# Kernel optimization log

Hardware: AMD Instinct MI355X
Metric: run time of the kernel (lower is better)

The kernel has to match this reference:

```python
import jax, jax.numpy as jnp
import numpy as np

B = 8          # batch
HID = 1024     # hidden_size
NH = 8         # query heads
KVH = 1        # kv heads (GQA)
HD = 256       # head_dim
NL = 18        # layers
MLP = 4096     # intermediate size
AH = 50        # action_horizon (suffix len)
AD = 32        # action_dim
P = 1037       # prefix_len
EPS = 1e-6
ROPE_BASE = 10000.0
SCALE = HD ** -0.5
NEG = -2.3819763e38


def _rms(x):
    return x * jax.lax.rsqrt(jnp.mean(x * x, axis=-1, keepdims=True) + EPS)


def _ada_norm(x, cond, W):
    # AdaRMS: cond -> (scale, shift, gate); normed*(1+scale)+shift, gate returned for gated residual
    scale, shift, gate = jnp.split(cond @ W, 3, axis=-1)
    return _rms(x) * (1.0 + scale[:, None, :]) + shift[:, None, :], gate[:, None, :]


def _rope(x, pos):
    # x: [B, heads, S, HD], pos: [B, S]; HF rotate-half convention
    inv = 1.0 / (ROPE_BASE ** (jnp.arange(0, HD, 2, dtype=jnp.float32) / HD))
    freqs = pos[:, :, None].astype(jnp.float32) * inv          # [B,S,HD/2]
    cos = jnp.tile(jnp.cos(freqs), (1, 1, 2))[:, None]          # [B,1,S,HD]
    sin = jnp.tile(jnp.sin(freqs), (1, 1, 2))[:, None]
    x1, x2 = jnp.split(x, 2, axis=-1)
    return x * cos + jnp.concatenate([-x2, x1], axis=-1) * sin


def setup_inputs() -> dict:
    key = jax.random.key(0)
    ks = jax.random.split(key, 24)
    s = 0.02
    return {
        'prefix_keys': jax.random.normal(ks[0], (B, NL, KVH, P, HD), jnp.float32),
        'prefix_values': jax.random.normal(ks[1], (B, NL, KVH, P, HD), jnp.float32),
        'prefix_pad_masks': jnp.ones((B, P), dtype=bool),
        'x_t': jax.random.normal(ks[2], (B, AH, AD), jnp.float32),
        'timestep': jax.random.uniform(ks[3], (B,), jnp.float32),
        'Wq': jax.random.normal(ks[4], (NL, HID, NH * HD), jnp.float32) * s,
        'Wk': jax.random.normal(ks[5], (NL, HID, KVH * HD), jnp.float32) * s,
        'Wv': jax.random.normal(ks[6], (NL, HID, KVH * HD), jnp.float32) * s,
        'Wo': jax.random.normal(ks[7], (NL, NH * HD, HID), jnp.float32) * s,
        'Wg': jax.random.normal(ks[8], (NL, HID, MLP), jnp.float32) * s,
        'Wu': jax.random.normal(ks[9], (NL, HID, MLP), jnp.float32) * s,
        'Wd': jax.random.normal(ks[10], (NL, MLP, HID), jnp.float32) * s,
        'A1': jax.random.normal(ks[11], (NL, HID, 3 * HID), jnp.float32) * s,
        'A2': jax.random.normal(ks[12], (NL, HID, 3 * HID), jnp.float32) * s,
        'Af': jax.random.normal(ks[13], (HID, 3 * HID), jnp.float32) * s,
        'W_act_in': jax.random.normal(ks[14], (AD, HID), jnp.float32) * s,
        'b_act_in': jnp.zeros((HID,), jnp.float32),
        'W_act_out': jax.random.normal(ks[15], (HID, AD), jnp.float32) * s,
        'b_act_out': jnp.zeros((AD,), jnp.float32),
        'W_t_in': jax.random.normal(ks[16], (HID, HID), jnp.float32) * s,
        'b_t_in': jnp.zeros((HID,), jnp.float32),
        'W_t_out': jax.random.normal(ks[17], (HID, HID), jnp.float32) * s,
        'b_t_out': jnp.zeros((HID,), jnp.float32),
    }


def reference(prefix_keys, prefix_values, prefix_pad_masks, x_t, timestep,
              Wq, Wk, Wv, Wo, Wg, Wu, Wd, A1, A2, Af,
              W_act_in, b_act_in, W_act_out, b_act_out,
              W_t_in, b_t_in, W_t_out, b_t_out):
    b = x_t.shape[0]
    # --- time embedding (sinusoidal over log-spaced periods) -> AdaRMS cond ---
    frac = jnp.linspace(0.0, 1.0, HID // 2)
    period = 0.004 * (4.0 / 0.004) ** frac
    sin_in = (2.0 * jnp.pi / period)[None, :] * timestep[:, None]
    temb = jnp.concatenate([jnp.sin(sin_in), jnp.cos(sin_in)], axis=1)  # [B,HID]
    cond = jax.nn.silu(jax.nn.silu(temb @ W_t_in + b_t_in) @ W_t_out + b_t_out)

    # --- action input projection ---
    h = x_t @ W_act_in + b_act_in  # [B,AH,HID]

    # --- attention mask & positions ---
    # suffix att_masks = [1,0,...,0] -> cumsum constant -> suffix block fully visible
    suf_att = jnp.ones((b, AH, AH), dtype=bool)
    s2p = jnp.broadcast_to(prefix_pad_masks[:, None, :], (b, AH, P))
    full = jnp.concatenate([s2p, suf_att], axis=2)          # [B,AH,P+AH]
    bias = jnp.where(full, 0.0, NEG).astype(jnp.float32)[:, None]  # [B,1,AH,P+AH]
    offs = jnp.sum(prefix_pad_masks.astype(jnp.int32), axis=-1, keepdims=True)
    pos = offs + jnp.arange(AH)                              # [B,AH]

    def layer(hcur, p):
        wq, wk, wv, wo, wg, wu, wd, a1, a2, ck, cv = p
        normed, gate = _ada_norm(hcur, cond, a1)
        q = (normed @ wq).reshape(b, AH, NH, HD).transpose(0, 2, 1, 3)
        k = (normed @ wk).reshape(b, AH, KVH, HD).transpose(0, 2, 1, 3)
        v = (normed @ wv).reshape(b, AH, KVH, HD).transpose(0, 2, 1, 3)
        q = _rope(q, pos)
        k = _rope(k, pos)
        fk = jnp.concatenate([ck, k], axis=2)   # [B,KVH,P+AH,HD]
        fv = jnp.concatenate([cv, v], axis=2)
        rep = NH // KVH
        fk = jnp.repeat(fk, rep, axis=1)
        fv = jnp.repeat(fv, rep, axis=1)
        scores = jnp.einsum('bhqd,bhkd->bhqk', q, fk) * SCALE + bias
        attn = jax.nn.softmax(scores, axis=-1)
        o = jnp.einsum('bhqk,bhkd->bhqd', attn, fv)
        o = o.transpose(0, 2, 1, 3).reshape(b, AH, NH * HD) @ wo
        h1 = hcur + gate * o                     # gated residual 1
        n2, gate2 = _ada_norm(h1, cond, a2)
        mlp = (jax.nn.gelu(n2 @ wg, approximate=True) * (n2 @ wu)) @ wd
        return h1 + gate2 * mlp, None            # gated residual 2

    pk = jnp.moveaxis(prefix_keys, 1, 0)   # [NL,B,KVH,P,HD]
    pv = jnp.moveaxis(prefix_values, 1, 0)
    h, _ = jax.lax.scan(layer, h, (Wq, Wk, Wv, Wo, Wg, Wu, Wd, A1, A2, pk, pv))

    out, _ = _ada_norm(h, cond, Af)
    return out @ W_act_out + b_act_out  # [B,AH,AD]
```

## Files before the change

kernel.cpp:

```cpp
#include <hip/hip_runtime.h>

typedef unsigned short u16;
typedef unsigned int   u32;
typedef __attribute__((ext_vector_type(8))) short bh8;
typedef __attribute__((ext_vector_type(4))) float f4;

constexpr int BATCH = 8, HIDN = 1024, NHEAD = 8, HD = 256, NLAY = 18, DMLP = 4096;
constexpr int AHOR = 50, ADIMN = 32, PFXN = 1037, SEQN = 1087, NSTR = 17, MR = 400, MP = 512;
constexpr float EPSV = 1e-6f, NEGV = -2.3819763e38f, QSCALE = 0.0625f;
constexpr size_t ADASL = (size_t)37 * 3 * BATCH * HIDN;

static __device__ __forceinline__ u16 f2bf(float x){
  union{float f; u32 u;} v; v.f = x;
  u32 r = (v.u + 0x7FFFu + ((v.u >> 16) & 1u)) >> 16;
  return (u16)r;
}
static __device__ __forceinline__ float bf2f(u16 u){
  union{u32 u; float f;} v; v.u = ((u32)u) << 16; return v.f;
}
static __device__ __forceinline__ u32 pack2(float a, float b){
  return (u32)f2bf(a) | ((u32)f2bf(b) << 16);
}
static __device__ __forceinline__ f4 MFMA(bh8 a, bh8 b, f4 c){
  return __builtin_amdgcn_mfma_f32_16x16x32_bf16(a, b, c, 0, 0, 0);
}
static __device__ __forceinline__ float siluf_(float x){ return x / (1.f + __expf(-x)); }
static __device__ __forceinline__ float geluf_(float x){
  float y = 0.7978845608028654f * (x + 0.044715f * x * x * x);
  float e = __expf(2.f * y);
  return 0.5f * x * (2.f - 2.f / (e + 1.f));
}

__global__ void k_prep(const int* __restrict__ mask, const float* __restrict__ ts,
                       float* __restrict__ temb, int* __restrict__ offs,
                       float* __restrict__ ropec, float* __restrict__ ropes)
{
  int t = threadIdx.x;
  {
    int b = t >> 5, l = t & 31;
    const int* mp = mask + b * PFXN;
    int s = 0;
    for (int k = l; k < PFXN; k += 32) s += (mp[k] != 0);
    #pragma unroll
    for (int off = 16; off >= 1; off >>= 1) s += __shfl_xor(s, off);
    if (l == 0) offs[b] = s;
  }
  for (int i = t; i < BATCH * 512; i += 256){
    int b = i >> 9, j = i & 511;
    float frac = (float)j * (1.0f / 511.0f);
    float period = 0.004f * __expf(frac * 6.907755278982137f);
    float arg = (6.283185307179586f / period) * ts[b];
    float s, c; sincosf(arg, &s, &c);
    temb[b * HIDN + j] = s;
    temb[b * HIDN + 512 + j] = c;
  }
  __syncthreads();
  for (int i = t; i < BATCH * AHOR * 128; i += 256){
    int d = i & 127, bt = i >> 7, b = bt / AHOR, tt = bt % AHOR;
    float inv = __expf(-((float)d * (1.f / 128.f)) * 9.210340371976184f);
    float arg = (float)(offs[b] + tt) * inv;
    float s, c; sincosf(arg, &s, &c);
    ropec[i] = c; ropes[i] = s;
  }
}

__global__ void k_tproj(const float* __restrict__ X, const float* __restrict__ W,
                        const float* __restrict__ bias, float* __restrict__ out)
{
  __shared__ float xs[BATCH * HIDN];
  __shared__ float red[BATCH][8][32];
  int t = threadIdx.x;
  for (int i = t; i < BATCH * HIDN; i += 256) xs[i] = X[i];
  __syncthreads();
  int c = t & 31, kp = t >> 5;
  int c0 = blockIdx.x * 32;
  float acc[BATCH];
  #pragma unroll
  for (int b = 0; b < BATCH; ++b) acc[b] = 0.f;
  for (int k = kp * 128; k < kp * 128 + 128; ++k){
    float w = W[(size_t)k * HIDN + c0 + c];
    #pragma unroll
    for (int b = 0; b < BATCH; ++b) acc[b] += xs[b * HIDN + k] * w;
  }
  #pragma unroll
  for (int b = 0; b < BATCH; ++b) red[b][kp][c] = acc[b];
  __syncthreads();
  int b2 = t >> 5, c2 = t & 31;
  float s = bias[c0 + c2];
  #pragma unroll
  for (int kp2 = 0; kp2 < 8; ++kp2) s += red[b2][kp2][c2];
  out[b2 * HIDN + c0 + c2] = siluf_(s);
}

__global__ void k_ada_part(const float* __restrict__ cond, const float* __restrict__ A1,
                           const float* __restrict__ A2, const float* __restrict__ Af,
                           float* __restrict__ adap)
{
  __shared__ float cs[BATCH * 256];
  int t = threadIdx.x;
  int y = blockIdx.y, ks = blockIdx.z;
  int k0 = ks * 256;
  for (int i = t; i < BATCH * 256; i += 256){
    int b = i >> 8, kk = i & 255;
    cs[i] = cond[b * HIDN + k0 + kk];
  }
  __syncthreads();
  const float* A = (y < NLAY) ? (A1 + (size_t)y * HIDN * 3072)
                  : (y < 2 * NLAY) ? (A2 + (size_t)(y - NLAY) * HIDN * 3072) : Af;
  int n = (blockIdx.x * 256 + t) * 4;
  f4 acc[BATCH];
  #pragma unroll
  for (int b = 0; b < BATCH; ++b) acc[b] = (f4){0.f,0.f,0.f,0.f};
  const float* ap = A + (size_t)k0 * 3072 + n;
  for (int kk = 0; kk < 256; kk += 8){
    f4 av[8];
    #pragma unroll
    for (int j = 0; j < 8; ++j) av[j] = *(const f4*)(ap + (size_t)(kk + j) * 3072);
    #pragma unroll
    for (int j = 0; j < 8; ++j){
      #pragma unroll
      for (int b = 0; b < BATCH; ++b) acc[b] += av[j] * cs[b * 256 + kk + j];
    }
  }
  int comp = n >> 10, nn = n & 1023;
  float* o = adap + (size_t)ks * ADASL + ((size_t)y * 3 + comp) * BATCH * HIDN + nn;
  #pragma unroll
  for (int b = 0; b < BATCH; ++b) *(f4*)(o + b * HIDN) = acc[b];
}

__global__ void k_ada_red(const float* __restrict__ adap, float* __restrict__ ada)
{
  size_t i = ((size_t)blockIdx.x * 256 + threadIdx.x) * 8;
  f4 a0 = {0,0,0,0}, a1 = {0,0,0,0};
  #pragma unroll
  for (int ks = 0; ks < 4; ++ks){
    const float* p = adap + (size_t)ks * ADASL + i;
    a0 += *(const f4*)p;
    a1 += *(const f4*)(p + 4);
  }
  *(f4*)(ada + i) = a0;
  *(f4*)(ada + i + 4) = a1;
}

__global__ void k_hin(const float* __restrict__ xt, const float* __restrict__ W,
                      const float* __restrict__ bias, float* __restrict__ h)
{
  int r = blockIdx.x;
  int t = threadIdx.x; int c0 = t * 4;
  __shared__ float xs[ADIMN];
  if (t < ADIMN) xs[t] = xt[r * ADIMN + t];
  __syncthreads();
  float a0 = bias[c0], a1 = bias[c0+1], a2 = bias[c0+2], a3 = bias[c0+3];
  for (int k = 0; k < ADIMN; ++k){
    float x = xs[k];
    const float* wp = W + k * HIDN + c0;
    a0 += x * wp[0]; a1 += x * wp[1]; a2 += x * wp[2]; a3 += x * wp[3];
  }
  float* hp = h + (size_t)r * HIDN + c0;
  hp[0] = a0; hp[1] = a1; hp[2] = a2; hp[3] = a3;
}

__global__ void k_resnorm(int mode, int np,
    const float* __restrict__ base, const u16* __restrict__ parts,
    const float* __restrict__ gate, const float* __restrict__ sc,
    const float* __restrict__ sh, float* __restrict__ outres,
    u16* __restrict__ fragA)
{
  __shared__ float redl[4];
  int t = threadIdx.x;
  int c = t * 4;
  for (int i = 0; i < 4; ++i){
    int r = blockIdx.x * 4 + i;
    bool live = (r < MR);
    float4 v = {0.f,0.f,0.f,0.f};
    int b = live ? (r / AHOR) : 0;
    if (live){
      v = *(const float4*)(base + (size_t)r * HIDN + c);
      if (mode){
        float s0 = 0, s1 = 0, s2 = 0, s3 = 0;
        #pragma unroll 4
        for (int p = 0; p < np; ++p){
          ushort4 u4 = *(const ushort4*)(parts + ((size_t)p * MP + r) * HIDN + c);
          s0 += bf2f(u4.x); s1 += bf2f(u4.y); s2 += bf2f(u4.z); s3 += bf2f(u4.w);
        }
        float4 gp = *(const float4*)(gate + b * HIDN + c);
        v.x += gp.x * s0; v.y += gp.y * s1; v.z += gp.z * s2; v.w += gp.w * s3;
        *(float4*)(outres + (size_t)r * HIDN + c) = v;
      }
    }
    float ss = v.x*v.x + v.y*v.y + v.z*v.z + v.w*v.w;
    #pragma unroll
    for (int off = 1; off < 64; off <<= 1) ss += __shfl_xor(ss, off);
    if ((t & 63) == 0) redl[t >> 6] = ss;
    __syncthreads();
    float tot = redl[0] + redl[1] + redl[2] + redl[3];
    __syncthreads();
    u16* dst = fragA + ((size_t)(c >> 3)) * MP * 8 + (size_t)r * 8 + (c & 7);
    ushort4 ov;
    if (live){
      float rstd = rsqrtf(tot * (1.0f / HIDN) + EPSV);
      const float4 scp = *(const float4*)(sc + b * HIDN + c);
      const float4 shp = *(const float4*)(sh + b * HIDN + c);
      ov.x = f2bf(v.x * rstd * (1.f + scp.x) + shp.x);
      ov.y = f2bf(v.y * rstd * (1.f + scp.y) + shp.y);
      ov.z = f2bf(v.z * rstd * (1.f + scp.z) + shp.z);
      ov.w = f2bf(v.w * rstd * (1.f + scp.w) + shp.w);
    } else {
      ov.x = ov.y = ov.z = ov.w = 0;
    }
    *(ushort4*)dst = ov;
  }
}

template<int NOUTER>
static __device__ __forceinline__ void gemm_core64(
    const u16* __restrict__ fa,
    const float* __restrict__ Wa, int cb0,
    const float* __restrict__ Wb, int cb1,
    int wN, int kc0, u16* lds, f4 acc[4][4])
{
  const int tid = threadIdx.x;
  const int lane = tid & 63, wave = tid >> 6;
  const int l15 = lane & 15, g = lane >> 4;
  const int wrow = wave * 64;
  const int sn = tid & 63, skb = (tid >> 6) * 8;
  const float* wbase = (sn < 32) ? (Wa + cb0 + sn) : (Wb + cb1 + (sn - 32));
  const size_t krow0 = (size_t)kc0 * 8 + skb;
  float pre[3][8];
  bh8 ab[2][2][4];
  #pragma unroll
  for (int j = 0; j < 8; ++j) pre[0][j] = wbase[(krow0 + j) * wN];
  #pragma unroll
  for (int kk = 0; kk < 2; ++kk){
    const u16* ap = fa + ((size_t)(kc0 + kk * 4 + g) * MP + wrow + l15) * 8;
    #pragma unroll
    for (int mf = 0; mf < 4; ++mf) ab[0][kk][mf] = *(const bh8*)(ap + mf * 128);
  }
  if (NOUTER > 1){
    #pragma unroll
    for (int j = 0; j < 8; ++j) pre[1][j] = wbase[(krow0 + 64 + j) * wN];
  }
  if (NOUTER > 2){
    #pragma unroll
    for (int j = 0; j < 8; ++j) pre[2][j] = wbase[(krow0 + 128 + j) * wN];
  }
  { u32* dst = (u32*)(lds + sn * 88 + skb);
    dst[0] = pack2(pre[0][0], pre[0][1]); dst[1] = pack2(pre[0][2], pre[0][3]);
    dst[2] = pack2(pre[0][4], pre[0][5]); dst[3] = pack2(pre[0][6], pre[0][7]); }
  __syncthreads();
  #pragma unroll
  for (int ko = 0; ko < NOUTER; ++ko){
    u16* ldsr = lds + (ko & 1) * (64 * 88);
    if (ko + 1 < NOUTER){
      #pragma unroll
      for (int kk = 0; kk < 2; ++kk){
        const u16* ap = fa + ((size_t)(kc0 + (ko + 1) * 8 + kk * 4 + g) * MP + wrow + l15) * 8;
        #pragma unroll
        for (int mf = 0; mf < 4; ++mf) ab[(ko + 1) & 1][kk][mf] = *(const bh8*)(ap + mf * 128);
      }
    }
    if (ko + 3 < NOUTER){
      #pragma unroll
      for (int j = 0; j < 8; ++j) pre[ko % 3][j] = wbase[(krow0 + (size_t)(ko + 3) * 64 + j) * wN];
    }
    #pragma unroll
    for (int kk = 0; kk < 2; ++kk){
      bh8 bb[4];
      #pragma unroll
      for (int nf = 0; nf < 4; ++nf) bb[nf] = *(const bh8*)(ldsr + (nf * 16 + l15) * 88 + kk * 32 + g * 8);
      #pragma unroll
      for (int mf = 0; mf < 4; ++mf)
        #pragma unroll
        for (int nf = 0; nf < 4; ++nf)
          acc[mf][nf] = MFMA(ab[ko & 1][kk][mf], bb[nf], acc[mf][nf]);
    }
    if (ko + 1 < NOUTER){
      u16* ldsw = lds + ((ko + 1) & 1) * (64 * 88);
      u32* dst = (u32*)(ldsw + sn * 88 + skb);
      const float* p = pre[(ko + 1) % 3];
      dst[0] = pack2(p[0], p[1]); dst[1] = pack2(p[2], p[3]);
      dst[2] = pack2(p[4], p[5]); dst[3] = pack2(p[6], p[7]);
      __syncthreads();
    }
  }
}

template<int NOUTER>
static __device__ __forceinline__ void gemm_core32w(
    const u16* __restrict__ fa,
    const float* __restrict__ Wa, int cb0,
    const float* __restrict__ Wb, int cb1,
    int wN, u16* lds, f4 acc[4][2])
{
  const int tid = threadIdx.x;
  const int lane = tid & 63, wave = tid >> 6;
  const int l15 = lane & 15, g = lane >> 4;
  const int wrow = wave * 64;
  const int sc = tid & 31, kq = tid >> 5;
  const int kb = kq * 8;
  const float* wbase = (sc < 16) ? (Wa + cb0 + sc) : (Wb + cb1 + (sc - 16));
  float pre[3][8];
  #pragma unroll
  for (int j = 0; j < 8; ++j) pre[0][j] = wbase[(size_t)(kb + j) * wN];
  if (NOUTER > 1){
    #pragma unroll
    for (int j = 0; j < 8; ++j) pre[1][j] = wbase[(size_t)(128 + kb + j) * wN];
  }
  if (NOUTER > 2){
    #pragma unroll
    for (int j = 0; j < 8; ++j) pre[2][j] = wbase[(size_t)(256 + kb + j) * wN];
  }
  { u32* dst = (u32*)(lds + sc * 136 + kb);
    dst[0] = pack2(pre[0][0], pre[0][1]); dst[1] = pack2(pre[0][2], pre[0][3]);
    dst[2] = pack2(pre[0][4], pre[0][5]); dst[3] = pack2(pre[0][6], pre[0][7]); }
  __syncthreads();
  #pragma unroll
  for (int ko = 0; ko < NOUTER; ++ko){
    u16* ldsr = lds + (ko & 1) * (32 * 136);
    bh8 a01[2][4], a23[2][4];
    #pragma unroll
    for (int kk = 0; kk < 2; ++kk){
      const u16* ap = fa + ((size_t)(ko * 16 + kk * 4 + g) * MP + wrow + l15) * 8;
      #pragma unroll
      for (int mf = 0; mf < 4; ++mf) a01[kk][mf] = *(const bh8*)(ap + mf * 128);
    }
    if (ko + 3 < NOUTER){
      #pragma unroll
      for (int j = 0; j < 8; ++j) pre[ko % 3][j] = wbase[(size_t)((ko + 3) * 128 + kb + j) * wN];
    }
    #pragma unroll
    for (int kk = 2; kk < 4; ++kk){
      const u16* ap = fa + ((size_t)(ko * 16 + kk * 4 + g) * MP + wrow + l15) * 8;
      #pragma unroll
      for (int mf = 0; mf < 4; ++mf) a23[kk - 2][mf] = *(const bh8*)(ap + mf * 128);
    }
    #pragma unroll
    for (int kk = 0; kk < 2; ++kk){
      bh8 bb[2];
      #pragma unroll
      for (int nf = 0; nf < 2; ++nf) bb[nf] = *(const bh8*)(ldsr + (nf * 16 + l15) * 136 + kk * 32 + g * 8);
      #pragma unroll
      for (int mf = 0; mf < 4; ++mf){
        acc[mf][0] = MFMA(a01[kk][mf], bb[0], acc[mf][0]);
        acc[mf][1] = MFMA(a01[kk][mf], bb[1], acc[mf][1]);
      }
    }
    #pragma unroll
    for (int kk = 2; kk < 4; ++kk){
      bh8 bb[2];
      #pragma unroll
      for (int nf = 0; nf < 2; ++nf) bb[nf] = *(const bh8*)(ldsr + (nf * 16 + l15) * 136 + kk * 32 + g * 8);
      #pragma unroll
      for (int mf = 0; mf < 4; ++mf){
        acc[mf][0] = MFMA(a23[kk - 2][mf], bb[0], acc[mf][0]);
        acc[mf][1] = MFMA(a23[kk - 2][mf], bb[1], acc[mf][1]);
      }
    }
    if (ko + 1 < NOUTER){
      u16* ldsw = lds + ((ko + 1) & 1) * (32 * 136);
      u32* dst = (u32*)(ldsw + sc * 136 + kb);
      const float* p = pre[(ko + 1) % 3];
      dst[0] = pack2(p[0], p[1]); dst[1] = pack2(p[2], p[3]);
      dst[2] = pack2(p[4], p[5]); dst[3] = pack2(p[6], p[7]);
      __syncthreads();
    }
  }
}

__global__ __launch_bounds__(512) void k_qkvrope(
    const u16* __restrict__ n1, const float* __restrict__ Wq,
    const float* __restrict__ Wk, const float* __restrict__ Wv,
    const float* __restrict__ ropec, const float* __restrict__ ropes,
    u16* __restrict__ qf, u16* __restrict__ ks, u16* __restrict__ vs)
{
  __shared__ u16 lds[2 * 64 * 88];
  int bx = blockIdx.x;
  const float* Wa; int cb0, cb1, wN, head = 0, d0 = 0, type;
  if (bx < 32){ type = 0; head = bx >> 2; d0 = (bx & 3) * 32; Wa = Wq; wN = NHEAD * HD; cb0 = head * HD + d0; cb1 = cb0 + 128; }
  else if (bx < 36){ type = 1; d0 = (bx - 32) * 32; Wa = Wk; wN = HD; cb0 = d0; cb1 = d0 + 128; }
  else { type = 2; d0 = (bx - 36) * 64; Wa = Wv; wN = HD; cb0 = d0; cb1 = cb0 + 32; }
  f4 acc[4][4];
  #pragma unroll
  for (int i = 0; i < 4; ++i)
    #pragma unroll
    for (int j = 0; j < 4; ++j) acc[i][j] = (f4){0.f, 0.f, 0.f, 0.f};
  gemm_core64<16>(n1, Wa, cb0, Wa, cb1, wN, 0, lds, acc);
  int tid = threadIdx.x, lane = tid & 63, wave = tid >> 6, l15 = lane & 15, g = lane >> 4;
  int wrow = wave * 64;
  #pragma unroll
  for (int mf = 0; mf < 4; ++mf)
    #pragma unroll
    for (int r = 0; r < 4; ++r){
      int row = wrow + mf * 16 + 4 * g + r;
      if (row >= MR) continue;
      int b = row / AHOR, tt = row - b * AHOR;
      if (type == 2){
        #pragma unroll
        for (int nf = 0; nf < 4; ++nf){
          int d = d0 + nf * 16 + l15;
          vs[((size_t)(b * AHOR + tt)) * HD + d] = f2bf(acc[mf][nf][r]);
        }
      } else {
        #pragma unroll
        for (int nf = 0; nf < 2; ++nf){
          int dA = d0 + nf * 16 + l15;
          float cz = ropec[(size_t)(b * AHOR + tt) * 128 + dA];
          float sz = ropes[(size_t)(b * AHOR + tt) * 128 + dA];
          float a = acc[mf][nf][r], bv = acc[mf][nf + 2][r];
          float oA = a * cz - bv * sz;
          float oB = bv * cz + a * sz;
          if (type == 0){
            oA *= QSCALE; oB *= QSCALE;
            int rowp = head * AHOR + tt;
            int dB = dA + 128;
            qf[((size_t)(b * 32 + (dA >> 3))) * MP * 8 + (size_t)rowp * 8 + (dA & 7)] = f2bf(oA);
            qf[((size_t)(b * 32 + (dB >> 3))) * MP * 8 + (size_t)rowp * 8 + (dB & 7)] = f2bf(oB);
          } else {
            size_t kb = ((size_t)(b * AHOR + tt)) * HD;
            ks[kb + dA] = f2bf(oA);
            ks[kb + dA + 128] = f2bf(oB);
          }
        }
      }
    }
}

__global__ __launch_bounds__(512) void k_attn(
    const u16* __restrict__ qf, const u16* __restrict__ kss, const u16* __restrict__ vss,
    const float* __restrict__ pk, const float* __restrict__ pv,
    const int* __restrict__ mask, int layer,
    u16* __restrict__ opart, float* __restrict__ mrow, float* __restrict__ lrow)
{
  __shared__ u16 kv[256 * 88];
  __shared__ u16 plds[MP * 72];
  int s = blockIdx.x, b = blockIdx.y;
  int tid = threadIdx.x, lane = tid & 63, wave = tid >> 6, l15 = lane & 15, g = lane >> 4;
  int wrow = wave * 64;
  int key = tid >> 3, dblk = (tid & 7) * 32;
  int kg = s * 64 + key;
  {
    u32* dst = (u32*)(kv + key * 264 + dblk);
    if (kg < PFXN){
      const float4* src = (const float4*)(pk + (((size_t)b * NLAY + layer) * PFXN + kg) * HD + dblk);
      #pragma unroll
      for (int j = 0; j < 8; ++j){ float4 v = src[j]; dst[2*j] = pack2(v.x, v.y); dst[2*j+1] = pack2(v.z, v.w); }
    } else if (kg < SEQN){
      const u32* src = (const u32*)(kss + ((size_t)b * AHOR + (kg - PFXN)) * HD + dblk);
      #pragma unroll
      for (int j = 0; j < 16; ++j) dst[j] = src[j];
    } else {
      #pragma unroll
      for (int j = 0; j < 16; ++j) dst[j] = 0;
    }
  }
  float vreg[32];
  if (kg < PFXN){
    const float4* src = (const float4*)(pv + (((size_t)b * NLAY + layer) * PFXN + kg) * HD + dblk);
    #pragma unroll
    for (int j = 0; j < 8; ++j){ float4 v = src[j]; vreg[4*j] = v.x; vreg[4*j+1] = v.y; vreg[4*j+2] = v.z; vreg[4*j+3] = v.w; }
  } else if (kg < SEQN){
    const u32* src = (const u32*)(vss + ((size_t)b * AHOR + (kg - PFXN)) * HD + dblk);
    #pragma unroll
    for (int j = 0; j < 16; ++j){ u32 u = src[j]; vreg[2*j] = bf2f((u16)(u & 0xFFFF)); vreg[2*j+1] = bf2f((u16)(u >> 16)); }
  } else {
    #pragma unroll
    for (int j = 0; j < 32; ++j) vreg[j] = 0.f;
  }
  bool valid[4];
  #pragma unroll
  for (int nf = 0; nf < 4; ++nf){
    int kgc = s * 64 + nf * 16 + l15;
    valid[nf] = (kgc < PFXN) ? (mask[b * PFXN + kgc] != 0) : (kgc < SEQN);
  }
  __syncthreads();
  f4 acc[4][4];
  #pragma unroll
  for (int i = 0; i < 4; ++i)
    #pragma unroll
    for (int j = 0; j < 4; ++j) acc[i][j] = (f4){0.f,0.f,0.f,0.f};
  const u16* qb = qf + (size_t)b * 32 * MP * 8;
  #pragma unroll
  for (int ko = 0; ko < 4; ++ko)
    #pragma unroll
    for (int kk = 0; kk < 2; ++kk){
      int kc = ko * 8 + kk * 4 + g;
      bh8 a[4], bb[4];
      const u16* ap = qb + ((size_t)kc * MP + wrow + l15) * 8;
      #pragma unroll
      for (int mf = 0; mf < 4; ++mf) a[mf] = *(const bh8*)(ap + mf * 128);
      #pragma unroll
      for (int nf = 0; nf < 4; ++nf) bb[nf] = *(const bh8*)(kv + (nf * 16 + l15) * 264 + ko * 64 + kk * 32 + g * 8);
      #pragma unroll
      for (int mf = 0; mf < 4; ++mf)
        #pragma unroll
        for (int nf = 0; nf < 4; ++nf) acc[mf][nf] = MFMA(a[mf], bb[nf], acc[mf][nf]);
    }
  #pragma unroll
  for (int nf = 0; nf < 4; ++nf) if (!valid[nf]){
    #pragma unroll
    for (int mf = 0; mf < 4; ++mf){
      acc[mf][nf][0] = NEGV; acc[mf][nf][1] = NEGV; acc[mf][nf][2] = NEGV; acc[mf][nf][3] = NEGV;
    }
  }
  #pragma unroll
  for (int mf = 0; mf < 4; ++mf)
    #pragma unroll
    for (int r = 0; r < 4; ++r){
      float m0 = fmaxf(fmaxf(acc[mf][0][r], acc[mf][1][r]), fmaxf(acc[mf][2][r], acc[mf][3][r]));
      #pragma unroll
      for (int off = 1; off < 16; off <<= 1) m0 = fmaxf(m0, __shfl_xor(m0, off));
      int row = wrow + mf * 16 + 4 * g + r;
      float sum = 0.f;
      #pragma unroll
      for (int nf = 0; nf < 4; ++nf){
        float p = __expf(acc[mf][nf][r] - m0);
        sum += p;
        plds[row * 72 + nf * 16 + l15] = f2bf(p);
      }
      #pragma unroll
      for (int off = 1; off < 16; off <<= 1) sum += __shfl_xor(sum, off);
      if (l15 == 0){
        mrow[((size_t)b * NSTR + s) * MP + row] = m0;
        lrow[((size_t)b * NSTR + s) * MP + row] = sum;
      }
    }
  __syncthreads();
  {
    #pragma unroll
    for (int j = 0; j < 32; ++j){
      int d = dblk + j;
      kv[d * 88 + ((d >> 5) & 3) * 8 + key] = f2bf(vreg[j]);
    }
  }
  __syncthreads();
  #pragma unroll
  for (int dc = 0; dc < 4; ++dc){
    f4 oc[4][4];
    #pragma unroll
    for (int i = 0; i < 4; ++i)
      #pragma unroll
      for (int j = 0; j < 4; ++j) oc[i][j] = (f4){0.f,0.f,0.f,0.f};
    #pragma unroll
    for (int kk = 0; kk < 2; ++kk){
      bh8 a[4], bb[4];
      #pragma unroll
      for (int mf = 0; mf < 4; ++mf) a[mf] = *(const bh8*)(plds + (wrow + mf * 16 + l15) * 72 + kk * 32 + g * 8);
      #pragma unroll
      for (int nf = 0; nf < 4; ++nf){
        int dcol = dc * 64 + nf * 16 + l15;
        bb[nf] = *(const bh8*)(kv + dcol * 88 + ((dcol >> 5) & 3) * 8 + kk * 32 + g * 8);
      }
      #pragma unroll
      for (int mf = 0; mf < 4; ++mf)
        #pragma unroll
        for (int nf = 0; nf < 4; ++nf) oc[mf][nf] = MFMA(a[mf], bb[nf], oc[mf][nf]);
    }
    #pragma unroll
    for (int mf = 0; mf < 4; ++mf)
      #pragma unroll
      for (int r = 0; r < 4; ++r){
        int row = wrow + mf * 16 + 4 * g + r;
        if (row < MR){
          #pragma unroll
          for (int nf = 0; nf < 4; ++nf){
            int d = dc * 64 + nf * 16 + l15;
            opart[(((size_t)b * NSTR + s) * MR + row) * HD + d] = f2bf(oc[mf][nf][r]);
          }
        }
      }
  }
}

__global__ void k_comb(const u16* __restrict__ opart, const float* __restrict__ mrow,
                       const float* __restrict__ lrow, u16* __restrict__ ao)
{
  int b = blockIdx.y;
  int d = threadIdx.x;
  int r0 = blockIdx.x * 16;
  for (int i = 0; i < 16; ++i){
    int row = r0 + i;
    float M = -3.0e38f;
    for (int s2 = 0; s2 < NSTR; ++s2) M = fmaxf(M, mrow[((size_t)b * NSTR + s2) * MP + row]);
    float L = 0.f, o = 0.f;
    for (int s2 = 0; s2 < NSTR; ++s2){
      float w = __expf(mrow[((size_t)b * NSTR + s2) * MP + row] - M);
      L += w * lrow[((size_t)b * NSTR + s2) * MP + row];
      o += w * bf2f(opart[(((size_t)b * NSTR + s2) * MR + row) * HD + d]);
    }
    float val = o / L;
    int h = row / AHOR, tt = row - h * AHOR;
    int col = h * HD + d;
    int rg = b * AHOR + tt;
    ao[((size_t)(col >> 3)) * MP * 8 + (size_t)rg * 8 + (col & 7)] = f2bf(val);
  }
}

template<int NOUTER>
__global__ __launch_bounds__(512) void k_gemm_part(
    const u16* __restrict__ fa, const float* __restrict__ W, int wN,
    int kcPerSlice, u16* __restrict__ outp)
{
  __shared__ u16 lds[2 * 64 * 88];
  int n0 = blockIdx.x * 64;
  int ksl = blockIdx.y;
  f4 acc[4][4];
  #pragma unroll
  for (int i = 0; i < 4; ++i)
    #pragma unroll
    for (int j = 0; j < 4; ++j) acc[i][j] = (f4){0.f,0.f,0.f,0.f};
  gemm_core64<NOUTER>(fa, W, n0, W, n0 + 32, wN, ksl * kcPerSlice, lds, acc);
  int tid = threadIdx.x, lane = tid & 63, wave = tid >> 6, l15 = lane & 15, g = lane >> 4;
  int wrow = wave * 64;
  #pragma unroll
  for (int mf = 0; mf < 4; ++mf)
    #pragma unroll
    for (int r = 0; r < 4; ++r){
      int row = wrow + mf * 16 + 4 * g + r;
      #pragma unroll
      for (int nf = 0; nf < 4; ++nf)
        outp[((size_t)ksl * MP + row) * 1024 + n0 + nf * 16 + l15] = f2bf(acc[mf][nf][r]);
    }
}

__global__ __launch_bounds__(512) void k_mlpup(
    const u16* __restrict__ n2, const float* __restrict__ Wg, const float* __restrict__ Wu,
    u16* __restrict__ mlpf)
{
  __shared__ u16 lds[2 * 32 * 136];
  int n0 = blockIdx.x * 16;
  f4 acc[4][2];
  #pragma unroll
  for (int i = 0; i < 4; ++i)
    #pragma unroll
    for (int j = 0; j < 2; ++j) acc[i][j] = (f4){0.f,0.f,0.f,0.f};
  gemm_core32w<8>(n2, Wg, n0, Wu, n0, DMLP, lds, acc);
  int tid = threadIdx.x, lane = tid & 63, wave = tid >> 6, l15 = lane & 15, g = lane >> 4;
  int wrow = wave * 64;
  #pragma unroll
  for (int mf = 0; mf < 4; ++mf)
    #pragma unroll
    for (int r = 0; r < 4; ++r){
      int row = wrow + mf * 16 + 4 * g + r;
      int col = n0 + l15;
      float gg = acc[mf][0][r], uu = acc[mf][1][r];
      float act = geluf_(gg) * uu;
      mlpf[((size_t)(col >> 3)) * MP * 8 + (size_t)row * 8 + (col & 7)] = f2bf(act);
    }
}

__global__ void k_out(const u16* __restrict__ nfr, const float* __restrict__ W,
                      const float* __restrict__ bias, float* __restrict__ out)
{
  int t = threadIdx.x;
  int row = blockIdx.x * 8 + (t >> 5);
  int c = t & 31;
  float acc = bias[c];
  for (int k = 0; k < HIDN; ++k)
    acc += bf2f(nfr[((size_t)(k >> 3)) * MP * 8 + (size_t)row * 8 + (k & 7)]) * W[k * ADIMN + c];
  out[row * ADIMN + c] = acc;
}

extern "C" void kernel_launch(void* const* d_in, const int* in_sizes, int n_in,
                              void* d_out, int out_size, void* d_ws, size_t ws_size,
                              hipStream_t stream)
{
  const float* pk  = (const float*)d_in[0];
  const float* pv  = (const float*)d_in[1];
  const int*   msk = (const int*)d_in[2];
  const float* xt  = (const float*)d_in[3];
  const float* ts  = (const float*)d_in[4];
  const float* Wq  = (const float*)d_in[5];
  const float* Wk  = (const float*)d_in[6];
  const float* Wv  = (const float*)d_in[7];
  const float* Wo  = (const float*)d_in[8];
  const float* Wg  = (const float*)d_in[9];
  const float* Wu  = (const float*)d_in[10];
  const float* Wd  = (const float*)d_in[11];
  const float* A1  = (const float*)d_in[12];
  const float* A2  = (const float*)d_in[13];
  const float* Af  = (const float*)d_in[14];
  const float* Wai = (const float*)d_in[15];
  const float* bai = (const float*)d_in[16];
  const float* Wao = (const float*)d_in[17];
  const float* bao = (const float*)d_in[18];
  const float* Wti = (const float*)d_in[19];
  const float* bti = (const float*)d_in[20];
  const float* Wto = (const float*)d_in[21];
  const float* bto = (const float*)d_in[22];

  char* w = (char*)d_ws;
  size_t off = 0;
  auto alloc = [&](size_t bytes) -> char* {
    char* p = w + off; off += (bytes + 255) & ~(size_t)255; return p;
  };
  float* temb  = (float*)alloc((size_t)BATCH * HIDN * 4);
  float* ttmp  = (float*)alloc((size_t)BATCH * HIDN * 4);
  float* cond  = (float*)alloc((size_t)BATCH * HIDN * 4);
  int*   offs  = (int*)alloc(BATCH * 4);
  float* ropec = (float*)alloc((size_t)BATCH * AHOR * 128 * 4);
  float* ropes = (float*)alloc((size_t)BATCH * AHOR * 128 * 4);
  float* ada   = (float*)alloc(ADASL * 4);
  float* adap  = (float*)alloc(4 * ADASL * 4);
  float* h     = (float*)alloc((size_t)MR * HIDN * 4);
  float* h1    = (float*)alloc((size_t)MR * HIDN * 4);
  u16*   n1    = (u16*)alloc((size_t)128 * MP * 8 * 2);
  u16*   n2    = (u16*)alloc((size_t)128 * MP * 8 * 2);
  u16*   qf    = (u16*)alloc((size_t)BATCH * 32 * MP * 8 * 2);
  u16*   kss   = (u16*)alloc((size_t)BATCH * AHOR * HD * 2);
  u16*   vss   = (u16*)alloc((size_t)BATCH * AHOR * HD * 2);
  u16*   opart = (u16*)alloc((size_t)BATCH * NSTR * MR * HD * 2);
  float* mrow  = (float*)alloc((size_t)BATCH * NSTR * MP * 4);
  float* lrow  = (float*)alloc((size_t)BATCH * NSTR * MP * 4);
  u16*   ao    = (u16*)alloc((size_t)256 * MP * 8 * 2);
  u16*   opp   = (u16*)alloc((size_t)8 * MP * 1024 * 2);
  u16*   mlpf  = (u16*)alloc((size_t)512 * MP * 8 * 2);
  u16*   mdp   = (u16*)alloc((size_t)8 * MP * 1024 * 2);
  if (off > ws_size) return;

  k_prep<<<1, 256, 0, stream>>>(msk, ts, temb, offs, ropec, ropes);
  k_tproj<<<32, 256, 0, stream>>>(temb, Wti, bti, ttmp);
  k_tproj<<<32, 256, 0, stream>>>(ttmp, Wto, bto, cond);
  k_ada_part<<<dim3(3, 37, 4), 256, 0, stream>>>(cond, A1, A2, Af, adap);
  k_ada_red<<<444, 256, 0, stream>>>(adap, ada);
  k_hin<<<MR, 256, 0, stream>>>(xt, Wai, bai, h);

  auto AP = [&](int y, int comp){ return ada + ((size_t)y * 3 + comp) * BATCH * HIDN; };

  k_resnorm<<<128, 256, 0, stream>>>(0, 0, h, nullptr, nullptr, AP(0,0), AP(0,1), nullptr, n1);

  for (int l = 0; l < NLAY; ++l){
    k_qkvrope<<<40, 512, 0, stream>>>(n1, Wq + (size_t)l * HIDN * NHEAD * HD,
                                      Wk + (size_t)l * HIDN * HD, Wv + (size_t)l * HIDN * HD,
                                      ropec, ropes, qf, kss, vss);
    k_attn<<<dim3(NSTR, BATCH), 512, 0, stream>>>(qf, kss, vss, pk, pv, msk, l, opart, mrow, lrow);
    k_comb<<<dim3(25, BATCH), 256, 0, stream>>>(opart, mrow, lrow, ao);
    k_gemm_part<4><<<dim3(16, 8), 512, 0, stream>>>(ao, Wo + (size_t)l * 2048 * 1024, 1024, 32, opp);
    k_resnorm<<<128, 256, 0, stream>>>(1, 8, h, opp, AP(l,2), AP(NLAY+l,0), AP(NLAY+l,1), h1, n2);
    k_mlpup<<<256, 512, 0, stream>>>(n2, Wg + (size_t)l * HIDN * DMLP, Wu + (size_t)l * HIDN * DMLP, mlpf);
    k_gemm_part<8><<<dim3(16, 8), 512, 0, stream>>>(mlpf, Wd + (size_t)l * DMLP * 1024, 1024, 64, mdp);
    const float* nsc = (l < NLAY - 1) ? AP(l + 1, 0) : AP(36, 0);
    const float* nsh = (l < NLAY - 1) ? AP(l + 1, 1) : AP(36, 1);
    k_resnorm<<<128, 256, 0, stream>>>(2, 8, h1, mdp, AP(NLAY+l,2), nsc, nsh, h, n1);
  }
  k_out<<<50, 256, 0, stream>>>(n1, Wao, bao, (float*)d_out);
}
```

Before: 3.532 ms.

## Split small kernels across more blocks to raise parallelism on the GPU

Several under-filled launches get more blocks. The ada-projection K-split goes from 4 to 8 parts. The QKV+RoPE GEMM goes from 40 to 80 blocks with narrower tiles via gemm_core32w. Attention is split over the head dimension in two z-halves, and the combine kernel goes from 25 to 100 blocks. The aim is better CU occupancy on a 256-CU device, at the cost of recomputing QK scores and softmax in both attention halves and loading K twice.

```diff
diff --git a/kernel.cpp b/kernel.cpp
--- a/kernel.cpp
+++ b/kernel.cpp
@@ -96,12 +96,12 @@
                            const float* __restrict__ A2, const float* __restrict__ Af,
                            float* __restrict__ adap)
 {
-  __shared__ float cs[BATCH * 256];
+  __shared__ float cs[BATCH * 128];
   int t = threadIdx.x;
   int y = blockIdx.y, ks = blockIdx.z;
-  int k0 = ks * 256;
-  for (int i = t; i < BATCH * 256; i += 256){
-    int b = i >> 8, kk = i & 255;
+  int k0 = ks * 128;
+  for (int i = t; i < BATCH * 128; i += 256){
+    int b = i >> 7, kk = i & 127;
     cs[i] = cond[b * HIDN + k0 + kk];
   }
   __syncthreads();
@@ -112,14 +112,14 @@
   #pragma unroll
   for (int b = 0; b < BATCH; ++b) acc[b] = (f4){0.f,0.f,0.f,0.f};
   const float* ap = A + (size_t)k0 * 3072 + n;
-  for (int kk = 0; kk < 256; kk += 8){
+  for (int kk = 0; kk < 128; kk += 8){
     f4 av[8];
     #pragma unroll
     for (int j = 0; j < 8; ++j) av[j] = *(const f4*)(ap + (size_t)(kk + j) * 3072);
     #pragma unroll
     for (int j = 0; j < 8; ++j){
       #pragma unroll
-      for (int b = 0; b < BATCH; ++b) acc[b] += av[j] * cs[b * 256 + kk + j];
+      for (int b = 0; b < BATCH; ++b) acc[b] += av[j] * cs[b * 128 + kk + j];
     }
   }
   int comp = n >> 10, nn = n & 1023;
@@ -133,7 +133,7 @@
   size_t i = ((size_t)blockIdx.x * 256 + threadIdx.x) * 8;
   f4 a0 = {0,0,0,0}, a1 = {0,0,0,0};
   #pragma unroll
-  for (int ks = 0; ks < 4; ++ks){
+  for (int ks = 0; ks < 8; ++ks){
     const float* p = adap + (size_t)ks * ADASL + i;
     a0 += *(const f4*)p;
     a1 += *(const f4*)(p + 4);
@@ -373,18 +373,18 @@
     const float* __restrict__ ropec, const float* __restrict__ ropes,
     u16* __restrict__ qf, u16* __restrict__ ks, u16* __restrict__ vs)
 {
-  __shared__ u16 lds[2 * 64 * 88];
+  __shared__ u16 lds[2 * 32 * 136];
   int bx = blockIdx.x;
-  const float* Wa; int cb0, cb1, wN, head = 0, d0 = 0, type;
-  if (bx < 32){ type = 0; head = bx >> 2; d0 = (bx & 3) * 32; Wa = Wq; wN = NHEAD * HD; cb0 = head * HD + d0; cb1 = cb0 + 128; }
-  else if (bx < 36){ type = 1; d0 = (bx - 32) * 32; Wa = Wk; wN = HD; cb0 = d0; cb1 = d0 + 128; }
-  else { type = 2; d0 = (bx - 36) * 64; Wa = Wv; wN = HD; cb0 = d0; cb1 = cb0 + 32; }
-  f4 acc[4][4];
+  const float *Wa, *Wb; int cb0, cb1, wN, type, head = 0, fb = 0, d0 = 0;
+  if (bx < 64){ type = 0; head = bx >> 3; fb = (bx & 7) * 16; Wa = Wq; Wb = Wq; wN = NHEAD * HD; cb0 = head * HD + fb; cb1 = cb0 + 128; }
+  else if (bx < 72){ type = 1; fb = (bx - 64) * 16; Wa = Wk; Wb = Wk; wN = HD; cb0 = fb; cb1 = fb + 128; }
+  else { type = 2; d0 = (bx - 72) * 32; Wa = Wv; Wb = Wv; wN = HD; cb0 = d0; cb1 = d0 + 16; }
+  f4 acc[4][2];
   #pragma unroll
   for (int i = 0; i < 4; ++i)
     #pragma unroll
-    for (int j = 0; j < 4; ++j) acc[i][j] = (f4){0.f, 0.f, 0.f, 0.f};
-  gemm_core64<16>(n1, Wa, cb0, Wa, cb1, wN, 0, lds, acc);
+    for (int j = 0; j < 2; ++j) acc[i][j] = (f4){0.f, 0.f, 0.f, 0.f};
+  gemm_core32w<8>(n1, Wa, cb0, Wb, cb1, wN, lds, acc);
   int tid = threadIdx.x, lane = tid & 63, wave = tid >> 6, l15 = lane & 15, g = lane >> 4;
   int wrow = wave * 64;
   #pragma unroll
@@ -394,32 +394,27 @@
       int row = wrow + mf * 16 + 4 * g + r;
       if (row >= MR) continue;
       int b = row / AHOR, tt = row - b * AHOR;
+      float lo = acc[mf][0][r], hi = acc[mf][1][r];
       if (type == 2){
-        #pragma unroll
-        for (int nf = 0; nf < 4; ++nf){
-          int d = d0 + nf * 16 + l15;
-          vs[((size_t)(b * AHOR + tt)) * HD + d] = f2bf(acc[mf][nf][r]);
-        }
+        size_t vb = ((size_t)(b * AHOR + tt)) * HD;
+        vs[vb + d0 + l15] = f2bf(lo);
+        vs[vb + d0 + 16 + l15] = f2bf(hi);
       } else {
-        #pragma unroll
-        for (int nf = 0; nf < 2; ++nf){
-          int dA = d0 + nf * 16 + l15;
-          float cz = ropec[(size_t)(b * AHOR + tt) * 128 + dA];
-          float sz = ropes[(size_t)(b * AHOR + tt) * 128 + dA];
-          float a = acc[mf][nf][r], bv = acc[mf][nf + 2][r];
-          float oA = a * cz - bv * sz;
-          float oB = bv * cz + a * sz;
-          if (type == 0){
-            oA *= QSCALE; oB *= QSCALE;
-            int rowp = head * AHOR + tt;
-            int dB = dA + 128;
-            qf[((size_t)(b * 32 + (dA >> 3))) * MP * 8 + (size_t)rowp * 8 + (dA & 7)] = f2bf(oA);
-            qf[((size_t)(b * 32 + (dB >> 3))) * MP * 8 + (size_t)rowp * 8 + (dB & 7)] = f2bf(oB);
-          } else {
-            size_t kb = ((size_t)(b * AHOR + tt)) * HD;
-            ks[kb + dA] = f2bf(oA);
-            ks[kb + dA + 128] = f2bf(oB);
-          }
+        int dA = fb + l15;
+        float cz = ropec[(size_t)(b * AHOR + tt) * 128 + dA];
+        float sz = ropes[(size_t)(b * AHOR + tt) * 128 + dA];
+        float oA = lo * cz - hi * sz;
+        float oB = hi * cz + lo * sz;
+        if (type == 0){
+          oA *= QSCALE; oB *= QSCALE;
+          int rowp = head * AHOR + tt;
+          int dB = dA + 128;
+          qf[((size_t)(b * 32 + (dA >> 3))) * MP * 8 + (size_t)rowp * 8 + (dA & 7)] = f2bf(oA);
+          qf[((size_t)(b * 32 + (dB >> 3))) * MP * 8 + (size_t)rowp * 8 + (dB & 7)] = f2bf(oB);
+        } else {
+          size_t kb = ((size_t)(b * AHOR + tt)) * HD;
+          ks[kb + dA] = f2bf(oA);
+          ks[kb + dA + 128] = f2bf(oB);
         }
       }
     }
@@ -431,14 +426,14 @@
     const int* __restrict__ mask, int layer,
     u16* __restrict__ opart, float* __restrict__ mrow, float* __restrict__ lrow)
 {
-  __shared__ u16 kv[256 * 88];
+  __shared__ u16 kv[64 * 264];
   __shared__ u16 plds[MP * 72];
-  int s = blockIdx.x, b = blockIdx.y;
+  int s = blockIdx.x, b = blockIdx.y, z = blockIdx.z;
   int tid = threadIdx.x, lane = tid & 63, wave = tid >> 6, l15 = lane & 15, g = lane >> 4;
   int wrow = wave * 64;
-  int key = tid >> 3, dblk = (tid & 7) * 32;
-  int kg = s * 64 + key;
   {
+    int key = tid >> 3, dblk = (tid & 7) * 32;
+    int kg = s * 64 + key;
     u32* dst = (u32*)(kv + key * 264 + dblk);
     if (kg < PFXN){
       const float4* src = (const float4*)(pk + (((size_t)b * NLAY + layer) * PFXN + kg) * HD + dblk);
@@ -454,17 +449,22 @@
     }
   }
   float vreg[32];
-  if (kg < PFXN){
-    const float4* src = (const float4*)(pv + (((size_t)b * NLAY + layer) * PFXN + kg) * HD + dblk);
-    #pragma unroll
-    for (int j = 0; j < 8; ++j){ float4 v = src[j]; vreg[4*j] = v.x; vreg[4*j+1] = v.y; vreg[4*j+2] = v.z; vreg[4*j+3] = v.w; }
-  } else if (kg < SEQN){
-    const u32* src = (const u32*)(vss + ((size_t)b * AHOR + (kg - PFXN)) * HD + dblk);
-    #pragma unroll
-    for (int j = 0; j < 16; ++j){ u32 u = src[j]; vreg[2*j] = bf2f((u16)(u & 0xFFFF)); vreg[2*j+1] = bf2f((u16)(u >> 16)); }
-  } else {
-    #pragma unroll
-    for (int j = 0; j < 32; ++j) vreg[j] = 0.f;
+  int vkey = tid >> 2, vdg = tid & 3;
+  if (tid < 256){
+    int kgv = s * 64 + vkey;
+    int vdb = z * 128 + vdg * 32;
+    if (kgv < PFXN){
+      const float4* src = (const float4*)(pv + (((size_t)b * NLAY + layer) * PFXN + kgv) * HD + vdb);
+      #pragma unroll
+      for (int j = 0; j < 8; ++j){ float4 v = src[j]; vreg[4*j] = v.x; vreg[4*j+1] = v.y; vreg[4*j+2] = v.z; vreg[4*j+3] = v.w; }
+    } else if (kgv < SEQN){
+      const u32* src = (const u32*)(vss + ((size_t)b * AHOR + (kgv - PFXN)) * HD + vdb);
+      #pragma unroll
+      for (int j = 0; j < 16; ++j){ u32 u = src[j]; vreg[2*j] = bf2f((u16)(u & 0xFFFF)); vreg[2*j+1] = bf2f((u16)(u >> 16)); }
+    } else {
+      #pragma unroll
+      for (int j = 0; j < 32; ++j) vreg[j] = 0.f;
+    }
   }
   bool valid[4];
   #pragma unroll
@@ -519,22 +519,22 @@
       }
       #pragma unroll
       for (int off = 1; off < 16; off <<= 1) sum += __shfl_xor(sum, off);
-      if (l15 == 0){
+      if (z == 0 && l15 == 0){
         mrow[((size_t)b * NSTR + s) * MP + row] = m0;
         lrow[((size_t)b * NSTR + s) * MP + row] = sum;
       }
     }
   __syncthreads();
-  {
+  if (tid < 256){
     #pragma unroll
     for (int j = 0; j < 32; ++j){
-      int d = dblk + j;
-      kv[d * 88 + ((d >> 5) & 3) * 8 + key] = f2bf(vreg[j]);
-    }
-  }
-  __syncthreads();
-  #pragma unroll
-  for (int dc = 0; dc < 4; ++dc){
+      int dloc = vdg * 32 + j;
+      kv[dloc * 88 + ((dloc >> 5) & 3) * 8 + vkey] = f2bf(vreg[j]);
+    }
+  }
+  __syncthreads();
+  #pragma unroll
+  for (int dcl = 0; dcl < 2; ++dcl){
     f4 oc[4][4];
     #pragma unroll
     for (int i = 0; i < 4; ++i)
@@ -547,8 +547,8 @@
       for (int mf = 0; mf < 4; ++mf) a[mf] = *(const bh8*)(plds + (wrow + mf * 16 + l15) * 72 + kk * 32 + g * 8);
       #pragma unroll
       for (int nf = 0; nf < 4; ++nf){
-        int dcol = dc * 64 + nf * 16 + l15;
-        bb[nf] = *(const bh8*)(kv + dcol * 88 + ((dcol >> 5) & 3) * 8 + kk * 32 + g * 8);
+        int dloc = dcl * 64 + nf * 16 + l15;
+        bb[nf] = *(const bh8*)(kv + dloc * 88 + ((dloc >> 5) & 3) * 8 + kk * 32 + g * 8);
       }
       #pragma unroll
       for (int mf = 0; mf < 4; ++mf)
@@ -563,7 +563,7 @@
         if (row < MR){
           #pragma unroll
           for (int nf = 0; nf < 4; ++nf){
-            int d = dc * 64 + nf * 16 + l15;
+            int d = z * 128 + dcl * 64 + nf * 16 + l15;
             opart[(((size_t)b * NSTR + s) * MR + row) * HD + d] = f2bf(oc[mf][nf][r]);
           }
         }
@@ -576,8 +576,8 @@
 {
   int b = blockIdx.y;
   int d = threadIdx.x;
-  int r0 = blockIdx.x * 16;
-  for (int i = 0; i < 16; ++i){
+  int r0 = blockIdx.x * 4;
+  for (int i = 0; i < 4; ++i){
     int row = r0 + i;
     float M = -3.0e38f;
     for (int s2 = 0; s2 < NSTR; ++s2) M = fmaxf(M, mrow[((size_t)b * NSTR + s2) * MP + row]);
@@ -700,7 +700,7 @@
   float* ropec = (float*)alloc((size_t)BATCH * AHOR * 128 * 4);
   float* ropes = (float*)alloc((size_t)BATCH * AHOR * 128 * 4);
   float* ada   = (float*)alloc(ADASL * 4);
-  float* adap  = (float*)alloc(4 * ADASL * 4);
+  float* adap  = (float*)alloc(8 * ADASL * 4);
   float* h     = (float*)alloc((size_t)MR * HIDN * 4);
   float* h1    = (float*)alloc((size_t)MR * HIDN * 4);
   u16*   n1    = (u16*)alloc((size_t)128 * MP * 8 * 2);
@@ -720,7 +720,7 @@
   k_prep<<<1, 256, 0, stream>>>(msk, ts, temb, offs, ropec, ropes);
   k_tproj<<<32, 256, 0, stream>>>(temb, Wti, bti, ttmp);
   k_tproj<<<32, 256, 0, stream>>>(ttmp, Wto, bto, cond);
-  k_ada_part<<<dim3(3, 37, 4), 256, 0, stream>>>(cond, A1, A2, Af, adap);
+  k_ada_part<<<dim3(3, 37, 8), 256, 0, stream>>>(cond, A1, A2, Af, adap);
   k_ada_red<<<444, 256, 0, stream>>>(adap, ada);
   k_hin<<<MR, 256, 0, stream>>>(xt, Wai, bai, h);
 
@@ -729,11 +729,11 @@
   k_resnorm<<<128, 256, 0, stream>>>(0, 0, h, nullptr, nullptr, AP(0,0), AP(0,1), nullptr, n1);
 
   for (int l = 0; l < NLAY; ++l){
-    k_qkvrope<<<40, 512, 0, stream>>>(n1, Wq + (size_t)l * HIDN * NHEAD * HD,
+    k_qkvrope<<<80, 512, 0, stream>>>(n1, Wq + (size_t)l * HIDN * NHEAD * HD,
                                       Wk + (size_t)l * HIDN * HD, Wv + (size_t)l * HIDN * HD,
                                       ropec, ropes, qf, kss, vss);
-    k_attn<<<dim3(NSTR, BATCH), 512, 0, stream>>>(qf, kss, vss, pk, pv, msk, l, opart, mrow, lrow);
-    k_comb<<<dim3(25, BATCH), 256, 0, stream>>>(opart, mrow, lrow, ao);
+    k_attn<<<dim3(NSTR, BATCH, 2), 512, 0, stream>>>(qf, kss, vss, pk, pv, msk, l, opart, mrow, lrow);
+    k_comb<<<dim3(100, BATCH), 256, 0, stream>>>(opart, mrow, lrow, ao);
     k_gemm_part<4><<<dim3(16, 8), 512, 0, stream>>>(ao, Wo + (size_t)l * 2048 * 1024, 1024, 32, opp);
     k_resnorm<<<128, 256, 0, stream>>>(1, 8, h, opp, AP(l,2), AP(NLAY+l,0), AP(NLAY+l,1), h1, n2);
     k_mlpup<<<256, 512, 0, stream>>>(n2, Wg + (size_t)l * HIDN * DMLP, Wu + (size_t)l * HIDN * DMLP, mlpf);
```

Measured after the change: 3.147 ms. -10.9%, faster.
